# Kernel tuning notes

Measured on AMD Instinct MI355X. Metric: run time of the kernel, lower is better.

The kernel has to match this reference:

```python
import math
import jax, jax.numpy as jnp
import numpy as np

NUM_HEADS = 16
N_WIRES = 8  # d_k, fixed by the quantum circuit
EMBED_DIM = NUM_HEADS * N_WIRES  # 128
BATCH = 4
SEQ = 2048


def setup_inputs() -> dict:
    key = jax.random.key(0)
    k1, k2, k3, k4 = jax.random.split(key, 4)
    x = jax.random.normal(k1, (BATCH, SEQ, EMBED_DIM), dtype=jnp.float32)
    theta = jax.random.normal(k2, (N_WIRES,), dtype=jnp.float32)
    Wc = jax.random.normal(k3, (EMBED_DIM, EMBED_DIM), dtype=jnp.float32) / math.sqrt(EMBED_DIM)
    bc = jax.random.normal(k4, (EMBED_DIM,), dtype=jnp.float32) * 0.01
    return {"x": x, "theta": theta, "Wc": Wc, "bc": bc}


def reference(x, theta, Wc, bc):
    # x: (B, S, E). Quantum layer: per (token, head), RX-encode the 8-dim slice,
    # apply trainable RX, measure PauliZ -> cos(x_i + theta_i) per wire (product state).
    B, S, E = x.shape
    H, dk = NUM_HEADS, N_WIRES
    proj = jnp.cos(x.reshape(B, S, H, dk) + theta)          # (B, S, H, dk)
    q = proj.transpose(0, 2, 1, 3)                          # (B, H, S, dk); q == k == v
    scale = 1.0 / math.sqrt(dk)
    scores = jnp.einsum('bhqd,bhkd->bhqk', q, q) * scale    # (B, H, S, S)
    attn = jax.nn.softmax(scores, axis=-1)                  # dropout p=0 (eval)
    out = jnp.einsum('bhqk,bhkd->bhqd', attn, q)            # (B, H, S, dk)
    merged = out.transpose(0, 2, 1, 3).reshape(B, S, E)     # (B, S, E)
    return merged @ Wc.T + bc                               # combine_heads Linear
```

## Files before the change

kernel.cpp:

```cpp
#include <hip/hip_runtime.h>
#include <math.h>

#define B_  4
#define S_  2048
#define H_  16
#define DK_ 8
#define E_  128

typedef _Float16 f16x8  __attribute__((ext_vector_type(8)));
typedef __fp16   h2     __attribute__((ext_vector_type(2)));
typedef float    f32x16 __attribute__((ext_vector_type(16)));
typedef int      i32x2  __attribute__((ext_vector_type(2)));

union U4  { unsigned u[4]; f16x8 v; uint4 q; };
union H2U { h2 h; unsigned u; };

#define KSC 0.51006972f

static __device__ __forceinline__ float fexp2(float x) {
#if __has_builtin(__builtin_amdgcn_exp2f)
    return __builtin_amdgcn_exp2f(x);
#else
    return __builtin_exp2f(x);
#endif
}

static __device__ __forceinline__ float frcp(float x) {
#if __has_builtin(__builtin_amdgcn_rcpf)
    return __builtin_amdgcn_rcpf(x);
#else
    return 1.0f / x;
#endif
}

__global__ __launch_bounds__(512, 4)
void qattn_mfma(const float* __restrict__ x, const float* __restrict__ theta,
                float* __restrict__ out) {
    constexpr int VST = 2056;
    __shared__ __align__(16) _Float16 smem[S_ * DK_ + 9 * VST];
    _Float16* Klds = smem;
    _Float16* Vt   = smem + S_ * DK_;

    const int tid  = threadIdx.x;
    const int lane = tid & 63;
    const int wv   = tid >> 6;
    const int bh   = blockIdx.y;
    const int b    = bh >> 4;
    const int h    = bh & 15;

    float th[DK_];
#pragma unroll
    for (int d = 0; d < DK_; ++d) th[d] = theta[d];

    const float* xp = x + ((size_t)b * S_) * E_ + h * DK_;
#pragma unroll
    for (int m = 0; m < 2; ++m) {
        const int s0 = tid * 4 + 2 * m;
        float4 a0 = *(const float4*)(xp + (size_t)s0 * E_);
        float4 a1 = *(const float4*)(xp + (size_t)s0 * E_ + 4);
        float4 b0 = *(const float4*)(xp + (size_t)(s0 + 1) * E_);
        float4 b1 = *(const float4*)(xp + (size_t)(s0 + 1) * E_ + 4);
        float ca[8], cb[8];
        ca[0]=__cosf(a0.x+th[0]); ca[1]=__cosf(a0.y+th[1]); ca[2]=__cosf(a0.z+th[2]); ca[3]=__cosf(a0.w+th[3]);
        ca[4]=__cosf(a1.x+th[4]); ca[5]=__cosf(a1.y+th[5]); ca[6]=__cosf(a1.z+th[6]); ca[7]=__cosf(a1.w+th[7]);
        cb[0]=__cosf(b0.x+th[0]); cb[1]=__cosf(b0.y+th[1]); cb[2]=__cosf(b0.z+th[2]); cb[3]=__cosf(b0.w+th[3]);
        cb[4]=__cosf(b1.x+th[4]); cb[5]=__cosf(b1.y+th[5]); cb[6]=__cosf(b1.z+th[6]); cb[7]=__cosf(b1.w+th[7]);

        H2U p0, p1, p2, p3;
        p0.h = __builtin_amdgcn_cvt_pkrtz(ca[0], ca[1]);
        p1.h = __builtin_amdgcn_cvt_pkrtz(ca[2], ca[3]);
        p2.h = __builtin_amdgcn_cvt_pkrtz(ca[4], ca[5]);
        p3.h = __builtin_amdgcn_cvt_pkrtz(ca[6], ca[7]);
        *(uint4*)&Klds[(size_t)s0 * DK_] = make_uint4(p0.u, p1.u, p2.u, p3.u);
        p0.h = __builtin_amdgcn_cvt_pkrtz(cb[0], cb[1]);
        p1.h = __builtin_amdgcn_cvt_pkrtz(cb[2], cb[3]);
        p2.h = __builtin_amdgcn_cvt_pkrtz(cb[4], cb[5]);
        p3.h = __builtin_amdgcn_cvt_pkrtz(cb[6], cb[7]);
        *(uint4*)&Klds[(size_t)(s0 + 1) * DK_] = make_uint4(p0.u, p1.u, p2.u, p3.u);

#pragma unroll
        for (int d = 0; d < DK_; ++d) {
            H2U tv; tv.h = __builtin_amdgcn_cvt_pkrtz(ca[d], cb[d]);
            *(unsigned*)&Vt[d * VST + s0] = tv.u;
        }
        *(unsigned*)&Vt[8 * VST + s0] = 0x3C003C00u;
    }
    __syncthreads();

    const int  qrow0 = blockIdx.x * 256 + wv * 32;
    const int  l31   = lane & 31;
    const int  hi    = lane >> 5;
    const bool lo32  = (lane < 32);

    f16x8 qf = {};
    if (lo32) {
        qf = *(const f16x8*)&Klds[(size_t)(qrow0 + l31) * DK_];
#pragma unroll
        for (int d = 0; d < DK_; ++d)
            qf[d] = qf[d] * (_Float16)KSC;
    }

    const f32x16 z16 = {};
    f32x16 accO = {};

    const int nc = (l31 <= 8) ? l31 : 8;
    const _Float16* vbase = &Vt[nc * VST + hi * 8];

#define LDK(T)    (*(const f16x8*)&Klds[(size_t)((((T) & 63) * 32) + l31) * DK_])
#define LDV(T, S) (*(const f16x8*)(vbase + (((T) & 63) * 32) + (S) * 16))

    f16x8 kfA  = LDK(0), kfB  = LDK(1);
    f16x8 vfA0 = LDV(0,0), vfA1 = LDV(0,1);
    f16x8 vfB0 = LDV(1,0), vfB1 = LDV(1,1);

#define TILE_BODY(KF, VF0, VF1, KTN)                                           \
    {                                                                          \
        f32x16 sc = __builtin_amdgcn_mfma_f32_32x32x16_f16(KF, qf, z16,0,0,0); \
        KF = LDK(KTN);                               \
        unsigned X[4][2];                                                      \
        _Pragma("unroll")                                                      \
        for (int q = 0; q < 4; ++q) {                                          \
            float w0 = fexp2(sc[4*q+0]);                                       \
            float w1 = fexp2(sc[4*q+1]);                                       \
            float w2 = fexp2(sc[4*q+2]);                                       \
            float w3 = fexp2(sc[4*q+3]);                                       \
            H2U p0, p1;                                                        \
            p0.h = __builtin_amdgcn_cvt_pkrtz(w0, w1);                         \
            p1.h = __builtin_amdgcn_cvt_pkrtz(w2, w3);                         \
            X[q][0] = p0.u; X[q][1] = p1.u;                                    \
        }                                                                      \
        _Pragma("unroll")                                                      \
        for (int s = 0; s < 2; ++s) {                                          \
            U4 pa;                                                             \
            _Pragma("unroll")                                                  \
            for (int i = 0; i < 2; ++i) {                                      \
                i32x2 r = __builtin_amdgcn_permlane32_swap(                    \
                    (int)X[2*s][i], (int)X[2*s+1][i], false, false);           \
                pa.u[i]     = (unsigned)r[0];                                  \
                pa.u[2 + i] = (unsigned)r[1];                                  \
            }                                                                  \
            accO = __builtin_amdgcn_mfma_f32_32x32x16_f16(                     \
                pa.v, (s == 0) ? VF0 : VF1, accO, 0, 0, 0);                    \
        }                                                                      \
        VF0 = LDV(KTN, 0); VF1 = LDV(KTN, 1);        \
    }

    for (int kt = 0; kt < S_ / 32; kt += 2) {
        TILE_BODY(kfA, vfA0, vfA1, kt + 2)
        TILE_BODY(kfB, vfB0, vfB1, kt + 3)
    }
#undef TILE_BODY
#undef LDK
#undef LDV

    const int n = l31;
    float* obase = out + ((size_t)(b * S_ + qrow0)) * E_ + h * DK_ + n;
#pragma unroll
    for (int i = 0; i < 16; ++i) {
        float den = __shfl(accO[i], (lane & 32) | 8, 64);
        float val = accO[i] * frcp(den);
        int row = (i & 3) + 8 * (i >> 2) + 4 * hi;
        if (n < DK_) obase[(size_t)row * E_] = val;
    }
}

__global__ __launch_bounds__(256, 2)
void proj_mfma(const float* __restrict__ Wc, const float* __restrict__ bc,
               float* __restrict__ io) {
    __shared__ __align__(16) _Float16 As[64 * E_];
    __shared__ __align__(16) _Float16 Bs[E_ * E_];
    const int tid  = threadIdx.x;
    const int lane = tid & 63;
    const int wv   = tid >> 6;
    const int l31  = lane & 31;
    const int hi   = lane >> 5;
    const int r0   = blockIdx.x * 64;

    for (int i = tid; i < 64 * 16; i += 256) {
        int r = i >> 4, c = i & 15;
        const float* s = io + (size_t)(r0 + r) * E_ + c * 8;
        float4 a = *(const float4*)s;
        float4 b = *(const float4*)(s + 4);
        H2U p0, p1, p2, p3;
        p0.h = __builtin_amdgcn_cvt_pkrtz(a.x, a.y);
        p1.h = __builtin_amdgcn_cvt_pkrtz(a.z, a.w);
        p2.h = __builtin_amdgcn_cvt_pkrtz(b.x, b.y);
        p3.h = __builtin_amdgcn_cvt_pkrtz(b.z, b.w);
        *(uint4*)&As[r * E_ + ((c ^ (r & 7)) * 8)] = make_uint4(p0.u, p1.u, p2.u, p3.u);
    }
    for (int i = tid; i < E_ * 16; i += 256) {
        int r = i >> 4, c = i & 15;
        const float* s = Wc + (size_t)r * E_ + c * 8;
        float4 a = *(const float4*)s;
        float4 b = *(const float4*)(s + 4);
        H2U p0, p1, p2, p3;
        p0.h = __builtin_amdgcn_cvt_pkrtz(a.x, a.y);
        p1.h = __builtin_amdgcn_cvt_pkrtz(a.z, a.w);
        p2.h = __builtin_amdgcn_cvt_pkrtz(b.x, b.y);
        p3.h = __builtin_amdgcn_cvt_pkrtz(b.z, b.w);
        *(uint4*)&Bs[r * E_ + ((c ^ (r & 7)) * 8)] = make_uint4(p0.u, p1.u, p2.u, p3.u);
    }
    __syncthreads();

    const int rg = wv & 1;
    const int cp = (wv >> 1) * 2;

    f32x16 acc0 = {}, acc1 = {};
    const f32x16 zz = {};
    (void)zz;
#pragma unroll
    for (int ks = 0; ks < 8; ++ks) {
        int ch = (ks * 2 + hi);
        f16x8 af  = *(const f16x8*)&As[(rg * 32 + l31) * E_ + ((ch ^ (l31 & 7)) * 8)];
        f16x8 bf0 = *(const f16x8*)&Bs[((cp + 0) * 32 + l31) * E_ + ((ch ^ (l31 & 7)) * 8)];
        f16x8 bf1 = *(const f16x8*)&Bs[((cp + 1) * 32 + l31) * E_ + ((ch ^ (l31 & 7)) * 8)];
        acc0 = __builtin_amdgcn_mfma_f32_32x32x16_f16(af, bf0, acc0, 0, 0, 0);
        acc1 = __builtin_amdgcn_mfma_f32_32x32x16_f16(af, bf1, acc1, 0, 0, 0);
    }

    const float b0 = bc[(cp + 0) * 32 + l31];
    const float b1 = bc[(cp + 1) * 32 + l31];
#pragma unroll
    for (int i = 0; i < 16; ++i) {
        int row = (i & 3) + 8 * (i >> 2) + 4 * hi;
        float* orow = io + (size_t)(r0 + rg * 32 + row) * E_;
        orow[(cp + 0) * 32 + l31] = acc0[i] + b0;
        orow[(cp + 1) * 32 + l31] = acc1[i] + b1;
    }
}

extern "C" void kernel_launch(void* const* d_in, const int* in_sizes, int n_in,
                              void* d_out, int out_size, void* d_ws, size_t ws_size,
                              hipStream_t stream) {
    const float* x     = (const float*)d_in[0];
    const float* theta = (const float*)d_in[1];
    const float* Wc    = (const float*)d_in[2];
    const float* bc    = (const float*)d_in[3];
    float* out = (float*)d_out;

    qattn_mfma<<<dim3(S_ / 256, B_ * H_), 512, 0, stream>>>(x, theta, out);
    proj_mfma<<<dim3((B_ * S_) / 64), 256, 0, stream>>>(Wc, bc, out);
}
```

Before: 47.78 us.

## Split key range across two wave groups per query tile and reduce via LDS

Doubles the attention block to 1024 threads: each query tile of 32 rows is now processed by two waves, each covering half of the keys, and the partial unnormalized outputs (including the denominator column) are summed through shared memory before normalization. The K/V staging loop is halved per thread accordingly. This raises wave-level parallelism and halves the serial MFMA/exp chain per wave, at the cost of extra syncs, an LDS reduction, and possibly lower achievable blocks per CU due to register/LDS limits.

```diff
diff --git a/kernel.cpp b/kernel.cpp
--- a/kernel.cpp
+++ b/kernel.cpp
@@ -33,7 +33,7 @@
 #endif
 }
 
-__global__ __launch_bounds__(512, 4)
+__global__ __launch_bounds__(1024, 8)
 void qattn_mfma(const float* __restrict__ x, const float* __restrict__ theta,
                 float* __restrict__ out) {
     constexpr int VST = 2056;
@@ -53,9 +53,8 @@
     for (int d = 0; d < DK_; ++d) th[d] = theta[d];
 
     const float* xp = x + ((size_t)b * S_) * E_ + h * DK_;
-#pragma unroll
-    for (int m = 0; m < 2; ++m) {
-        const int s0 = tid * 4 + 2 * m;
+    {
+        const int s0 = tid * 2;
         float4 a0 = *(const float4*)(xp + (size_t)s0 * E_);
         float4 a1 = *(const float4*)(xp + (size_t)s0 * E_ + 4);
         float4 b0 = *(const float4*)(xp + (size_t)(s0 + 1) * E_);
@@ -87,7 +86,10 @@
     }
     __syncthreads();
 
-    const int  qrow0 = blockIdx.x * 256 + wv * 32;
+    const int  qg    = wv & 7;
+    const int  kh    = wv >> 3;
+    const int  qrow0 = blockIdx.x * 256 + qg * 32;
+    const int  t0    = kh * 32;
     const int  l31   = lane & 31;
     const int  hi    = lane >> 5;
     const bool lo32  = (lane < 32);
@@ -109,9 +111,9 @@
 #define LDK(T)    (*(const f16x8*)&Klds[(size_t)((((T) & 63) * 32) + l31) * DK_])
 #define LDV(T, S) (*(const f16x8*)(vbase + (((T) & 63) * 32) + (S) * 16))
 
-    f16x8 kfA  = LDK(0), kfB  = LDK(1);
-    f16x8 vfA0 = LDV(0,0), vfA1 = LDV(0,1);
-    f16x8 vfB0 = LDV(1,0), vfB1 = LDV(1,1);
+    f16x8 kfA  = LDK(t0),     kfB  = LDK(t0 + 1);
+    f16x8 vfA0 = LDV(t0, 0),  vfA1 = LDV(t0, 1);
+    f16x8 vfB0 = LDV(t0+1,0), vfB1 = LDV(t0+1,1);
 
 #define TILE_BODY(KF, VF0, VF1, KTN)                                           \
     {                                                                          \
@@ -145,7 +147,7 @@
         VF0 = LDV(KTN, 0); VF1 = LDV(KTN, 1);        \
     }
 
-    for (int kt = 0; kt < S_ / 32; kt += 2) {
+    for (int kt = t0; kt < t0 + 32; kt += 2) {
         TILE_BODY(kfA, vfA0, vfA1, kt + 2)
         TILE_BODY(kfB, vfB0, vfB1, kt + 3)
     }
@@ -153,14 +155,33 @@
 #undef LDK
 #undef LDV
 
-    const int n = l31;
-    float* obase = out + ((size_t)(b * S_ + qrow0)) * E_ + h * DK_ + n;
-#pragma unroll
-    for (int i = 0; i < 16; ++i) {
-        float den = __shfl(accO[i], (lane & 32) | 8, 64);
-        float val = accO[i] * frcp(den);
-        int row = (i & 3) + 8 * (i >> 2) + 4 * hi;
-        if (n < DK_) obase[(size_t)row * E_] = val;
+    __syncthreads();
+    float* scratch = (float*)smem;
+    if (kh == 1) {
+        float4* dst = (float4*)&scratch[(size_t)(qg * 64 + lane) * 16];
+#pragma unroll
+        for (int i = 0; i < 4; ++i)
+            dst[i] = make_float4(accO[4*i], accO[4*i+1], accO[4*i+2], accO[4*i+3]);
+    }
+    __syncthreads();
+    if (kh == 0) {
+        const float4* src = (const float4*)&scratch[(size_t)(qg * 64 + lane) * 16];
+#pragma unroll
+        for (int i = 0; i < 4; ++i) {
+            float4 p = src[i];
+            accO[4*i+0] += p.x; accO[4*i+1] += p.y;
+            accO[4*i+2] += p.z; accO[4*i+3] += p.w;
+        }
+
+        const int n = l31;
+        float* obase = out + ((size_t)(b * S_ + qrow0)) * E_ + h * DK_ + n;
+#pragma unroll
+        for (int i = 0; i < 16; ++i) {
+            float den = __shfl(accO[i], (lane & 32) | 8, 64);
+            float val = accO[i] * frcp(den);
+            int row = (i & 3) + 8 * (i >> 2) + 4 * hi;
+            if (n < DK_) obase[(size_t)row * E_] = val;
+        }
     }
 }
 
@@ -206,8 +227,6 @@
     const int cp = (wv >> 1) * 2;
 
     f32x16 acc0 = {}, acc1 = {};
-    const f32x16 zz = {};
-    (void)zz;
 #pragma unroll
     for (int ks = 0; ks < 8; ++ks) {
         int ch = (ks * 2 + hi);
@@ -238,6 +257,6 @@
     const float* bc    = (const float*)d_in[3];
     float* out = (float*)d_out;
 
-    qattn_mfma<<<dim3(S_ / 256, B_ * H_), 512, 0, stream>>>(x, theta, out);
+    qattn_mfma<<<dim3(S_ / 256, B_ * H_), 1024, 0, stream>>>(x, theta, out);
     proj_mfma<<<dim3((B_ * S_) / 64), 256, 0, stream>>>(Wc, bc, out);
 }
```

Measured after the change: 66.08 us. +38.3%, slower.

## Software-pipeline score MFMA one tile ahead and split PV accumulator

Applied to the files above, without the earlier changes.

Restructures the attention inner loop so the QK^T MFMA for tile kt+2 is issued right after the exp2 of the current tile's scores. This lets the score MFMA overlap the exp/convert/permlane work instead of the exp waiting on a freshly issued MFMA. The PV accumulation is split into two independent accumulators, summed at the end, to break the serial MFMA dependency chain. Register prefetch of K/V fragments is dropped in favour of direct LDS loads, and the last two tiles are peeled. This raises accumulator register pressure and may reduce occupancy.

```diff
diff --git a/kernel.cpp b/kernel.cpp
--- a/kernel.cpp
+++ b/kernel.cpp
@@ -48,42 +48,44 @@
     const int b    = bh >> 4;
     const int h    = bh & 15;
 
-    float th[DK_];
-#pragma unroll
-    for (int d = 0; d < DK_; ++d) th[d] = theta[d];
-
-    const float* xp = x + ((size_t)b * S_) * E_ + h * DK_;
-#pragma unroll
-    for (int m = 0; m < 2; ++m) {
-        const int s0 = tid * 4 + 2 * m;
-        float4 a0 = *(const float4*)(xp + (size_t)s0 * E_);
-        float4 a1 = *(const float4*)(xp + (size_t)s0 * E_ + 4);
-        float4 b0 = *(const float4*)(xp + (size_t)(s0 + 1) * E_);
-        float4 b1 = *(const float4*)(xp + (size_t)(s0 + 1) * E_ + 4);
-        float ca[8], cb[8];
-        ca[0]=__cosf(a0.x+th[0]); ca[1]=__cosf(a0.y+th[1]); ca[2]=__cosf(a0.z+th[2]); ca[3]=__cosf(a0.w+th[3]);
-        ca[4]=__cosf(a1.x+th[4]); ca[5]=__cosf(a1.y+th[5]); ca[6]=__cosf(a1.z+th[6]); ca[7]=__cosf(a1.w+th[7]);
-        cb[0]=__cosf(b0.x+th[0]); cb[1]=__cosf(b0.y+th[1]); cb[2]=__cosf(b0.z+th[2]); cb[3]=__cosf(b0.w+th[3]);
-        cb[4]=__cosf(b1.x+th[4]); cb[5]=__cosf(b1.y+th[5]); cb[6]=__cosf(b1.z+th[6]); cb[7]=__cosf(b1.w+th[7]);
-
-        H2U p0, p1, p2, p3;
-        p0.h = __builtin_amdgcn_cvt_pkrtz(ca[0], ca[1]);
-        p1.h = __builtin_amdgcn_cvt_pkrtz(ca[2], ca[3]);
-        p2.h = __builtin_amdgcn_cvt_pkrtz(ca[4], ca[5]);
-        p3.h = __builtin_amdgcn_cvt_pkrtz(ca[6], ca[7]);
-        *(uint4*)&Klds[(size_t)s0 * DK_] = make_uint4(p0.u, p1.u, p2.u, p3.u);
-        p0.h = __builtin_amdgcn_cvt_pkrtz(cb[0], cb[1]);
-        p1.h = __builtin_amdgcn_cvt_pkrtz(cb[2], cb[3]);
-        p2.h = __builtin_amdgcn_cvt_pkrtz(cb[4], cb[5]);
-        p3.h = __builtin_amdgcn_cvt_pkrtz(cb[6], cb[7]);
-        *(uint4*)&Klds[(size_t)(s0 + 1) * DK_] = make_uint4(p0.u, p1.u, p2.u, p3.u);
-
-#pragma unroll
-        for (int d = 0; d < DK_; ++d) {
-            H2U tv; tv.h = __builtin_amdgcn_cvt_pkrtz(ca[d], cb[d]);
-            *(unsigned*)&Vt[d * VST + s0] = tv.u;
+    {
+        float th[DK_];
+#pragma unroll
+        for (int d = 0; d < DK_; ++d) th[d] = theta[d];
+
+        const float* xp = x + ((size_t)b * S_) * E_ + h * DK_;
+#pragma unroll
+        for (int m = 0; m < 2; ++m) {
+            const int s0 = tid * 4 + 2 * m;
+            float4 a0 = *(const float4*)(xp + (size_t)s0 * E_);
+            float4 a1 = *(const float4*)(xp + (size_t)s0 * E_ + 4);
+            float4 b0 = *(const float4*)(xp + (size_t)(s0 + 1) * E_);
+            float4 b1 = *(const float4*)(xp + (size_t)(s0 + 1) * E_ + 4);
+            float ca[8], cb[8];
+            ca[0]=__cosf(a0.x+th[0]); ca[1]=__cosf(a0.y+th[1]); ca[2]=__cosf(a0.z+th[2]); ca[3]=__cosf(a0.w+th[3]);
+            ca[4]=__cosf(a1.x+th[4]); ca[5]=__cosf(a1.y+th[5]); ca[6]=__cosf(a1.z+th[6]); ca[7]=__cosf(a1.w+th[7]);
+            cb[0]=__cosf(b0.x+th[0]); cb[1]=__cosf(b0.y+th[1]); cb[2]=__cosf(b0.z+th[2]); cb[3]=__cosf(b0.w+th[3]);
+            cb[4]=__cosf(b1.x+th[4]); cb[5]=__cosf(b1.y+th[5]); cb[6]=__cosf(b1.z+th[6]); cb[7]=__cosf(b1.w+th[7]);
+
+            H2U p0, p1, p2, p3;
+            p0.h = __builtin_amdgcn_cvt_pkrtz(ca[0], ca[1]);
+            p1.h = __builtin_amdgcn_cvt_pkrtz(ca[2], ca[3]);
+            p2.h = __builtin_amdgcn_cvt_pkrtz(ca[4], ca[5]);
+            p3.h = __builtin_amdgcn_cvt_pkrtz(ca[6], ca[7]);
+            *(uint4*)&Klds[(size_t)s0 * DK_] = make_uint4(p0.u, p1.u, p2.u, p3.u);
+            p0.h = __builtin_amdgcn_cvt_pkrtz(cb[0], cb[1]);
+            p1.h = __builtin_amdgcn_cvt_pkrtz(cb[2], cb[3]);
+            p2.h = __builtin_amdgcn_cvt_pkrtz(cb[4], cb[5]);
+            p3.h = __builtin_amdgcn_cvt_pkrtz(cb[6], cb[7]);
+            *(uint4*)&Klds[(size_t)(s0 + 1) * DK_] = make_uint4(p0.u, p1.u, p2.u, p3.u);
+
+#pragma unroll
+            for (int d = 0; d < DK_; ++d) {
+                H2U tv; tv.h = __builtin_amdgcn_cvt_pkrtz(ca[d], cb[d]);
+                *(unsigned*)&Vt[d * VST + s0] = tv.u;
+            }
+            *(unsigned*)&Vt[8 * VST + s0] = 0x3C003C00u;
         }
-        *(unsigned*)&Vt[8 * VST + s0] = 0x3C003C00u;
     }
     __syncthreads();
 
@@ -101,57 +103,73 @@
     }
 
     const f32x16 z16 = {};
-    f32x16 accO = {};
+    f32x16 accP = {}, accQ = {};
 
     const int nc = (l31 <= 8) ? l31 : 8;
     const _Float16* vbase = &Vt[nc * VST + hi * 8];
 
-#define LDK(T)    (*(const f16x8*)&Klds[(size_t)((((T) & 63) * 32) + l31) * DK_])
-#define LDV(T, S) (*(const f16x8*)(vbase + (((T) & 63) * 32) + (S) * 16))
-
-    f16x8 kfA  = LDK(0), kfB  = LDK(1);
-    f16x8 vfA0 = LDV(0,0), vfA1 = LDV(0,1);
-    f16x8 vfB0 = LDV(1,0), vfB1 = LDV(1,1);
-
-#define TILE_BODY(KF, VF0, VF1, KTN)                                           \
+#define LDK(T)    (*(const f16x8*)&Klds[(size_t)(((T) * 32) + l31) * DK_])
+#define LDV(T, S) (*(const f16x8*)(vbase + ((T) * 32) + (S) * 16))
+
+#define PROC(SC, T, TN, REFILL)                                                \
     {                                                                          \
-        f32x16 sc = __builtin_amdgcn_mfma_f32_32x32x16_f16(KF, qf, z16,0,0,0); \
-        KF = LDK(KTN);                               \
         unsigned X[4][2];                                                      \
         _Pragma("unroll")                                                      \
         for (int q = 0; q < 4; ++q) {                                          \
-            float w0 = fexp2(sc[4*q+0]);                                       \
-            float w1 = fexp2(sc[4*q+1]);                                       \
-            float w2 = fexp2(sc[4*q+2]);                                       \
-            float w3 = fexp2(sc[4*q+3]);                                       \
+            float w0 = fexp2(SC[4*q+0]);                                       \
+            float w1 = fexp2(SC[4*q+1]);                                       \
+            float w2 = fexp2(SC[4*q+2]);                                       \
+            float w3 = fexp2(SC[4*q+3]);                                       \
             H2U p0, p1;                                                        \
             p0.h = __builtin_amdgcn_cvt_pkrtz(w0, w1);                         \
             p1.h = __builtin_amdgcn_cvt_pkrtz(w2, w3);                         \
             X[q][0] = p0.u; X[q][1] = p1.u;                                    \
         }                                                                      \
-        _Pragma("unroll")                                                      \
-        for (int s = 0; s < 2; ++s) {                                          \
+        if (REFILL)                                                            \
+            SC = __builtin_amdgcn_mfma_f32_32x32x16_f16(LDK(TN), qf, z16,      \
+                                                        0, 0, 0);              \
+        {                                                                      \
             U4 pa;                                                             \
             _Pragma("unroll")                                                  \
             for (int i = 0; i < 2; ++i) {                                      \
                 i32x2 r = __builtin_amdgcn_permlane32_swap(                    \
-                    (int)X[2*s][i], (int)X[2*s+1][i], false, false);           \
+                    (int)X[0][i], (int)X[1][i], false, false);                 \
                 pa.u[i]     = (unsigned)r[0];                                  \
                 pa.u[2 + i] = (unsigned)r[1];                                  \
             }                                                                  \
-            accO = __builtin_amdgcn_mfma_f32_32x32x16_f16(                     \
-                pa.v, (s == 0) ? VF0 : VF1, accO, 0, 0, 0);                    \
+            accP = __builtin_amdgcn_mfma_f32_32x32x16_f16(                     \
+                pa.v, LDV(T, 0), accP, 0, 0, 0);                               \
         }                                                                      \
-        VF0 = LDV(KTN, 0); VF1 = LDV(KTN, 1);        \
-    }
-
-    for (int kt = 0; kt < S_ / 32; kt += 2) {
-        TILE_BODY(kfA, vfA0, vfA1, kt + 2)
-        TILE_BODY(kfB, vfB0, vfB1, kt + 3)
-    }
-#undef TILE_BODY
+        {                                                                      \
+            U4 pa;                                                             \
+            _Pragma("unroll")                                                  \
+            for (int i = 0; i < 2; ++i) {                                      \
+                i32x2 r = __builtin_amdgcn_permlane32_swap(                    \
+                    (int)X[2][i], (int)X[3][i], false, false);                 \
+                pa.u[i]     = (unsigned)r[0];                                  \
+                pa.u[2 + i] = (unsigned)r[1];                                  \
+            }                                                                  \
+            accQ = __builtin_amdgcn_mfma_f32_32x32x16_f16(                     \
+                pa.v, LDV(T, 1), accQ, 0, 0, 0);                               \
+        }                                                                      \
+    }
+
+    f32x16 scA = __builtin_amdgcn_mfma_f32_32x32x16_f16(LDK(0), qf, z16, 0, 0, 0);
+    f32x16 scB = __builtin_amdgcn_mfma_f32_32x32x16_f16(LDK(1), qf, z16, 0, 0, 0);
+
+    for (int kt = 0; kt < 62; kt += 2) {
+        PROC(scA, kt,     kt + 2, 1)
+        PROC(scB, kt + 1, kt + 3, 1)
+    }
+    PROC(scA, 62, 0, 0)
+    PROC(scB, 63, 0, 0)
+#undef PROC
 #undef LDK
 #undef LDV
+
+    f32x16 accO;
+#pragma unroll
+    for (int i = 0; i < 16; ++i) accO[i] = accP[i] + accQ[i];
 
     const int n = l31;
     float* obase = out + ((size_t)(b * S_ + qrow0)) * E_ + h * DK_ + n;
@@ -206,8 +224,6 @@
     const int cp = (wv >> 1) * 2;
 
     f32x16 acc0 = {}, acc1 = {};
-    const f32x16 zz = {};
-    (void)zz;
 #pragma unroll
     for (int ks = 0; ks < 8; ++ks) {
         int ch = (ks * 2 + hi);
```

Result: faster. 46.18 us (-3.3%).
